# Performance work log

Hardware: AMD Instinct MI355X
Metric: run time of the kernel (lower is better)

## Reference

```python
import jax, jax.numpy as jnp
import numpy as np
from jax import lax

PATCH = 16
DILATIONS = (1, 2, 4, 8)
R2_THRESH = 0.5


def setup_inputs() -> dict:
    key = jax.random.key(0)
    k1, k2, k3 = jax.random.split(key, 3)
    seasonal = jax.random.normal(k1, (32, 2048, 8), dtype=jnp.float32)
    # 4 Conv1d(1,1,k=16) kernels + biases (PyTorch default init scale ~1/sqrt(k))
    conv_w = jax.random.normal(k2, (4, PATCH), dtype=jnp.float32) / np.sqrt(PATCH).astype(np.float32)
    conv_b = jax.random.normal(k3, (4,), dtype=jnp.float32) * 0.01
    return {"seasonal": seasonal, "conv_w": conv_w, "conv_b": conv_b}


def _r2(y):
    n = y.shape[-1]
    x = jnp.arange(n, dtype=y.dtype)
    xm = x - x.mean()                                  # [2p]
    ym = y - y.mean(axis=-1, keepdims=True)            # [..., 2p]
    sxy = jnp.einsum('...k,k->...', ym, xm)
    sxx = jnp.sum(xm * xm)
    syy = jnp.sum(ym * ym, axis=-1)
    return (sxy * sxy) / (sxx * syy)


def _forward(seasonal, conv_w, conv_b):
    B, S, C = seasonal.shape
    p = PATCH
    # channels are processed independently with the SAME convs -> fuse B and C
    x = seasonal.transpose(0, 2, 1).reshape(B * C, 1, S)  # [BC,1,S]
    win = jnp.arange(S - p + 1)[:, None] + jnp.arange(p)[None, :]  # [n_patches,p]
    cand_list = []
    for i, d in enumerate(DILATIONS):
        pad = (p - 1) * d
        out = lax.conv_general_dilated(
            x, conv_w[i].reshape(1, 1, p), window_strides=(1,),
            padding=[(pad, pad)], rhs_dilation=(d,)) + conv_b[i]
        out = out[:, 0, :S]                      # crop to seq_len, [BC,S]
        cand_list.append(out[:, win])            # sliding windows [BC,n_patches,p]
    cand = jnp.concatenate(cand_list, axis=1)    # [BC,N,p]
    N = cand.shape[1]

    # r^2 score for every adjacent pair (vectorized; greedy scan only gates it)
    pair = jnp.concatenate([cand[:, :-1], cand[:, 1:]], axis=-1)  # [BC,N-1,2p]
    can_merge = jnp.pad(_r2(pair) >= R2_THRESH, ((0, 0), (0, 1)),
                        constant_values=False)   # [BC,N]; last idx never merges

    # greedy sequential merge: if pair (i,i+1) merges, i+1 is consumed
    def step(consumed, cm_i):
        merge = jnp.logical_and(~consumed, cm_i)
        return merge, (merge, ~consumed)

    def scan_one(cm):
        _, (merge, valid) = lax.scan(step, jnp.zeros((), jnp.bool_), cm)
        return merge, valid

    merge, valid = jax.vmap(scan_one)(can_merge)  # [BC,N] each

    nxt = jnp.concatenate([cand[:, 1:], cand[:, -1:]], axis=1)
    outs = jnp.where(merge[..., None], 0.5 * (cand + nxt), cand)  # [BC,N,p]

    # pack selected patches to the front (stable order), zero-pad the tail
    order = jnp.argsort(~valid, axis=1)  # jax argsort is stable; valid first
    packed = jnp.take_along_axis(outs, order[..., None], axis=1)
    vmask = jnp.take_along_axis(valid, order, axis=1)
    packed = packed * vmask[..., None].astype(packed.dtype)

    return packed.reshape(B, C, N, p).transpose(0, 2, 3, 1)  # [B,N,p,C]


def reference(seasonal, conv_w, conv_b):
    return _forward(seasonal, conv_w, conv_b)
```

## Files before the change

### kernel.cpp

```cpp
#include <hip/hip_runtime.h>

#define SLEN 2048
#define PATCH 16
#define ND 4
#define NW 2033
#define NCAND 8132
#define NROWS 256
#define NCH 8
#define ROWPAD 8192


__global__ __launch_bounds__(256) void k_conv(
    const float* __restrict__ seasonal,
    const float* __restrict__ conv_w,
    const float* __restrict__ conv_b,
    double* __restrict__ convd,
    float* __restrict__ convf)
{
    const int bid = blockIdx.x;
    const int row = bid >> 2;
    const int d   = bid & 3;
    const int dil = 1 << d;
    const int b = row >> 3, c = row & 7;

    __shared__ float xs[SLEN];
    #pragma unroll
    for (int j = 0; j < SLEN/256; ++j) {
        int s = threadIdx.x + j*256;
        xs[s] = seasonal[(size_t)(b*SLEN + s)*NCH + c];
    }
    double w[PATCH];
    #pragma unroll
    for (int k = 0; k < PATCH; ++k) w[k] = (double)conv_w[d*PATCH + k];
    const double bias = (double)conv_b[d];
    __syncthreads();

    const size_t obase = ((size_t)row*ND + d)*SLEN;
    #pragma unroll
    for (int j = 0; j < SLEN/256; ++j) {
        int t = threadIdx.x + j*256;
        double acc = 0.0;
        #pragma unroll
        for (int k = 0; k < PATCH; ++k) {
            int idx = t - (PATCH-1-k)*dil;
            if (idx >= 0) acc += w[k] * (double)xs[idx];
        }
        acc += bias;
        convd[obase + t] = acc;
        convf[obase + t] = (float)acc;
    }
}

__global__ __launch_bounds__(256) void k_cm(
    const double* __restrict__ convd,
    unsigned char* __restrict__ cmb)
{
    const int row = blockIdx.x >> 2;
    const int d   = blockIdx.x & 3;
    const int tid = threadIdx.x;
    const double* g = convd + ((size_t)row*ND + d)*SLEN;
    unsigned char* crow = cmb + (size_t)row*ROWPAD + d*NW;

    if (tid < 254) {
        const int w0 = tid*8;
        double W1=0.0, W2=0.0, Wk=0.0;
        #pragma unroll
        for (int k = 0; k < 16; ++k) {
            double v = g[w0+k];
            W1 += v; W2 = fma(v,v,W2); Wk = fma((double)k,v,Wk);
        }
        unsigned char bits[8];
        #pragma unroll
        for (int j = 0; j < 8; ++j) {
            double v0 = g[w0+j], v16 = g[w0+j+16];
            double nW1 = W1 + (v16 - v0);
            double nW2 = W2 + (v16*v16 - v0*v0);
            double nWk = Wk - W1 + v0 + 15.0*v16;
            double S1  = W1 + nW1;
            double S2  = W2 + nW2;
            double Sxy = (Wk - 15.5*W1) + (nWk + 0.5*nW1);
            double syy = S2 - S1*S1*(1.0/32.0);
            bits[j] = (unsigned char)((Sxy*Sxy >= 1364.0*syy) && (syy > 0.0));
            W1 = nW1; W2 = nW2; Wk = nWk;
        }
        #pragma unroll
        for (int j = 0; j < 8; ++j) crow[w0+j] = bits[j];
    } else if (tid == 254 && d < 3) {
        const double* g2 = convd + ((size_t)row*ND + d + 1)*SLEN;
        double aW1=0,aW2=0,aWk=0, bW1=0,bW2=0,bWk=0;
        #pragma unroll
        for (int k = 0; k < 16; ++k) {
            double va = g[2032+k]; aW1 += va; aW2 = fma(va,va,aW2); aWk = fma((double)k,va,aWk);
            double vb = g2[k];     bW1 += vb; bW2 = fma(vb,vb,bW2); bWk = fma((double)k,vb,bWk);
        }
        double S1  = aW1 + bW1;
        double S2  = aW2 + bW2;
        double Sxy = (aWk - 15.5*aW1) + (bWk + 0.5*bW1);
        double syy = S2 - S1*S1*(1.0/32.0);
        crow[2032] = (unsigned char)((Sxy*Sxy >= 1364.0*syy) && (syy > 0.0));
    }
}

__global__ __launch_bounds__(256) void k_pack(
    const unsigned char* __restrict__ cmb,
    int* __restrict__ sel)
{
    const int row = blockIdx.x;
    const int tid = threadIdx.x;
    __shared__ unsigned char c0out[256];
    __shared__ int pmax[256];
    __shared__ unsigned sums[256];

    const unsigned* cmw = (const unsigned*)(cmb + (size_t)row*ROWPAD);
    unsigned cmbits = 0;
    #pragma unroll
    for (int q = 0; q < 8; ++q) {
        unsigned wrd = cmw[tid*8 + q];
        #pragma unroll
        for (int bb = 0; bb < 4; ++bb) {
            int p = tid*32 + q*4 + bb;
            unsigned bit = ((wrd >> (8*bb)) & 0xffu) ? 1u : 0u;
            if (p >= NCAND-1) bit = 0;
            cmbits |= bit << (q*4 + bb);
        }
    }

    unsigned inv = ~cmbits;
    unsigned T = (inv == 0u) ? 32u : (unsigned)__clz(inv);
    c0out[tid] = (unsigned char)(T & 1u);
    pmax[tid]  = (inv == 0u) ? -1 : tid;
    __syncthreads();
    for (int off = 1; off < 256; off <<= 1) {
        int v = (tid >= off) ? pmax[tid-off] : -1;
        __syncthreads();
        if (v > pmax[tid]) pmax[tid] = v;
        __syncthreads();
    }
    unsigned carry = 0;
    if (tid > 0) { int m = pmax[tid-1]; if (m >= 0) carry = c0out[m]; }

    unsigned cons = carry;
    unsigned validb = 0, mergeb = 0;
    int cnt = 0;
    const int base = tid*32;
    int nelem = NCAND - base; if (nelem > 32) nelem = 32; if (nelem < 0) nelem = 0;
    for (int w = 0; w < nelem; ++w) {
        unsigned bit = (cmbits >> w) & 1u;
        unsigned val = cons ^ 1u;
        unsigned mrg = bit & val;
        validb |= val << w;
        mergeb |= mrg << w;
        cnt += (int)val;
        cons = mrg;
    }

    sums[tid] = (unsigned)cnt;
    __syncthreads();
    for (int off = 1; off < 256; off <<= 1) {
        unsigned v = (tid >= off) ? sums[tid-off] : 0u;
        __syncthreads();
        sums[tid] += v;
        __syncthreads();
    }
    unsigned r = sums[tid] - (unsigned)cnt;
    unsigned total = sums[255];
    int* selrow = sel + (size_t)row*ROWPAD;
    for (int w = 0; w < nelem; ++w) {
        if ((validb >> w) & 1u)
            selrow[r++] = ((base + w) << 1) | (int)((mergeb >> w) & 1u);
    }
    for (int idx = (int)total + tid; idx < ROWPAD; idx += 256)
        selrow[idx] = -1;
}

__global__ __launch_bounds__(256) void k_out(
    const float* __restrict__ convf,
    const int* __restrict__ sel,
    float* __restrict__ out)
{
    __shared__ float tile[32*132];
    const int t = threadIdx.x;
    const int c = t & 7;
    const int s = t >> 3;
    const unsigned slab = blockIdx.x*32u + (unsigned)s;
    const unsigned b = slab / NCAND;
    const unsigned n = slab - b*NCAND;
    const unsigned row = b*NCH + (unsigned)c;

    const int e = sel[(size_t)row*ROWPAD + n];
    float vals[16];
    if (e < 0) {
        #pragma unroll
        for (int k = 0; k < 16; ++k) vals[k] = 0.0f;
    } else {
        const int i = e >> 1;
        const int d = (i >= 3*NW) ? 3 : (i >= 2*NW) ? 2 : (i >= NW) ? 1 : 0;
        const float* cf = convf + (size_t)row*8192 + i + 15*d;
        float f[17];
        #pragma unroll
        for (int k = 0; k < 17; ++k) f[k] = cf[k];
        if (e & 1) {
            const int i2 = i + 1;
            const int d2 = (i2 >= 3*NW) ? 3 : (i2 >= 2*NW) ? 2 : (i2 >= NW) ? 1 : 0;
            if (d2 != d) {
                const float* cg = convf + (size_t)row*8192 + i2 + 15*d2;
                #pragma unroll
                for (int k = 0; k < 16; ++k) vals[k] = 0.5f*(f[k] + cg[k]);
            } else {
                #pragma unroll
                for (int k = 0; k < 16; ++k) vals[k] = 0.5f*(f[k] + f[k+1]);
            }
        } else {
            #pragma unroll
            for (int k = 0; k < 16; ++k) vals[k] = f[k];
        }
    }
    float* tr = tile + s*132 + c;
    #pragma unroll
    for (int k = 0; k < 16; ++k) tr[k*8] = vals[k];
    __syncthreads();

    const size_t obase = (size_t)blockIdx.x * 4096;
    #pragma unroll
    for (int m = 0; m < 4; ++m) {
        int L  = (t + m*256)*4;
        int s2 = L >> 7, j = L & 127;
        float4 v = *(const float4*)&tile[s2*132 + j];
        *(float4*)&out[obase + L] = v;
    }
}

extern "C" void kernel_launch(void* const* d_in, const int* in_sizes, int n_in,
                              void* d_out, int out_size, void* d_ws, size_t ws_size,
                              hipStream_t stream) {
    const float* seasonal = (const float*)d_in[0];
    const float* conv_w   = (const float*)d_in[1];
    const float* conv_b   = (const float*)d_in[2];
    float* out = (float*)d_out;

    char* ws = (char*)d_ws;
    double*        convd = (double*)(ws);
    float*         convf = (float*)(ws + 16777216);
    unsigned char* cmb   = (unsigned char*)(ws + 25165824);
    int*           sel   = (int*)(ws);

    hipLaunchKernelGGL(k_conv, dim3(NROWS*ND), dim3(256), 0, stream,
                       seasonal, conv_w, conv_b, convd, convf);
    hipLaunchKernelGGL(k_cm,   dim3(NROWS*ND), dim3(256), 0, stream,
                       convd, cmb);
    hipLaunchKernelGGL(k_pack, dim3(NROWS), dim3(256), 0, stream,
                       cmb, sel);
    hipLaunchKernelGGL(k_out,  dim3(8132), dim3(256), 0, stream,
                       convf, sel, out);
}
```

Before: 177.8 us.

## Fuse conv, r2 mask and pack kernels into one per-row front kernel

Merges the convolution, the r^2 merge-flag computation and the greedy pack scan into a single kernel with one block per row. The double-precision conv output now stays in padded shared memory instead of a global buffer, and the byte mask also lives in shared memory. This drops two launches and the global double and byte-mask round trips. In exchange the grid shrinks from 1024 to 256 blocks, so each block runs the four dilations one after another with more syncs and much more shared memory, which may lower occupancy.

```diff
diff --git a/kernel.cpp b/kernel.cpp
--- a/kernel.cpp
+++ b/kernel.cpp
@@ -10,108 +10,99 @@
 #define ROWPAD 8192
 
 
-__global__ __launch_bounds__(256) void k_conv(
+#define CDI5(x) ((x) + ((x) >> 5))
+
+__global__ __launch_bounds__(256) void k_front(
     const float* __restrict__ seasonal,
     const float* __restrict__ conv_w,
     const float* __restrict__ conv_b,
-    double* __restrict__ convd,
-    float* __restrict__ convf)
-{
-    const int bid = blockIdx.x;
-    const int row = bid >> 2;
-    const int d   = bid & 3;
-    const int dil = 1 << d;
-    const int b = row >> 3, c = row & 7;
-
-    __shared__ float xs[SLEN];
-    #pragma unroll
-    for (int j = 0; j < SLEN/256; ++j) {
-        int s = threadIdx.x + j*256;
-        xs[s] = seasonal[(size_t)(b*SLEN + s)*NCH + c];
-    }
-    double w[PATCH];
-    #pragma unroll
-    for (int k = 0; k < PATCH; ++k) w[k] = (double)conv_w[d*PATCH + k];
-    const double bias = (double)conv_b[d];
-    __syncthreads();
-
-    const size_t obase = ((size_t)row*ND + d)*SLEN;
-    #pragma unroll
-    for (int j = 0; j < SLEN/256; ++j) {
-        int t = threadIdx.x + j*256;
-        double acc = 0.0;
-        #pragma unroll
-        for (int k = 0; k < PATCH; ++k) {
-            int idx = t - (PATCH-1-k)*dil;
-            if (idx >= 0) acc += w[k] * (double)xs[idx];
-        }
-        acc += bias;
-        convd[obase + t] = acc;
-        convf[obase + t] = (float)acc;
-    }
-}
-
-__global__ __launch_bounds__(256) void k_cm(
-    const double* __restrict__ convd,
-    unsigned char* __restrict__ cmb)
-{
-    const int row = blockIdx.x >> 2;
-    const int d   = blockIdx.x & 3;
-    const int tid = threadIdx.x;
-    const double* g = convd + ((size_t)row*ND + d)*SLEN;
-    unsigned char* crow = cmb + (size_t)row*ROWPAD + d*NW;
-
-    if (tid < 254) {
-        const int w0 = tid*8;
-        double W1=0.0, W2=0.0, Wk=0.0;
-        #pragma unroll
-        for (int k = 0; k < 16; ++k) {
-            double v = g[w0+k];
-            W1 += v; W2 = fma(v,v,W2); Wk = fma((double)k,v,Wk);
-        }
-        unsigned char bits[8];
-        #pragma unroll
-        for (int j = 0; j < 8; ++j) {
-            double v0 = g[w0+j], v16 = g[w0+j+16];
-            double nW1 = W1 + (v16 - v0);
-            double nW2 = W2 + (v16*v16 - v0*v0);
-            double nWk = Wk - W1 + v0 + 15.0*v16;
-            double S1  = W1 + nW1;
-            double S2  = W2 + nW2;
-            double Sxy = (Wk - 15.5*W1) + (nWk + 0.5*nW1);
-            double syy = S2 - S1*S1*(1.0/32.0);
-            bits[j] = (unsigned char)((Sxy*Sxy >= 1364.0*syy) && (syy > 0.0));
-            W1 = nW1; W2 = nW2; Wk = nWk;
-        }
-        #pragma unroll
-        for (int j = 0; j < 8; ++j) crow[w0+j] = bits[j];
-    } else if (tid == 254 && d < 3) {
-        const double* g2 = convd + ((size_t)row*ND + d + 1)*SLEN;
-        double aW1=0,aW2=0,aWk=0, bW1=0,bW2=0,bWk=0;
-        #pragma unroll
-        for (int k = 0; k < 16; ++k) {
-            double va = g[2032+k]; aW1 += va; aW2 = fma(va,va,aW2); aWk = fma((double)k,va,aWk);
-            double vb = g2[k];     bW1 += vb; bW2 = fma(vb,vb,bW2); bWk = fma((double)k,vb,bWk);
-        }
-        double S1  = aW1 + bW1;
-        double S2  = aW2 + bW2;
-        double Sxy = (aWk - 15.5*aW1) + (bWk + 0.5*bW1);
-        double syy = S2 - S1*S1*(1.0/32.0);
-        crow[2032] = (unsigned char)((Sxy*Sxy >= 1364.0*syy) && (syy > 0.0));
-    }
-}
-
-__global__ __launch_bounds__(256) void k_pack(
-    const unsigned char* __restrict__ cmb,
+    float* __restrict__ convf,
     int* __restrict__ sel)
 {
     const int row = blockIdx.x;
+    const int b = row >> 3, c = row & 7;
     const int tid = threadIdx.x;
+
+    __shared__ float xs[SLEN];
+    __shared__ double cdd[CDI5(SLEN-1)+1];
+    __shared__ double prevtail[16];
+    __shared__ unsigned char cma[8192];
     __shared__ unsigned char c0out[256];
     __shared__ int pmax[256];
     __shared__ unsigned sums[256];
 
-    const unsigned* cmw = (const unsigned*)(cmb + (size_t)row*ROWPAD);
+    #pragma unroll
+    for (int j = 0; j < 8; ++j) {
+        int s = tid + j*256;
+        xs[s] = seasonal[(size_t)(b*SLEN + s)*NCH + c];
+    }
+    __syncthreads();
+
+    for (int d = 0; d < ND; ++d) {
+        double w[PATCH];
+        #pragma unroll
+        for (int k = 0; k < PATCH; ++k) w[k] = (double)conv_w[d*PATCH + k];
+        const double bias = (double)conv_b[d];
+        const int dil = 1 << d;
+        #pragma unroll
+        for (int j = 0; j < 8; ++j) {
+            int t = tid + j*256;
+            double acc = 0.0;
+            #pragma unroll
+            for (int k = 0; k < PATCH; ++k) {
+                int idx = t - (PATCH-1-k)*dil;
+                if (idx >= 0) acc += w[k] * (double)xs[idx];
+            }
+            acc += bias;
+            cdd[CDI5(t)] = acc;
+            convf[(size_t)row*8192 + d*SLEN + t] = (float)acc;
+        }
+        __syncthreads();
+
+        if (tid < 254) {
+            const int w0 = tid*8;
+            double W1=0.0, W2=0.0, Wk=0.0;
+            #pragma unroll
+            for (int k = 0; k < 16; ++k) {
+                double v = cdd[CDI5(w0+k)];
+                W1 += v; W2 = fma(v,v,W2); Wk = fma((double)k,v,Wk);
+            }
+            unsigned char* crow = cma + d*NW;
+            #pragma unroll
+            for (int j = 0; j < 8; ++j) {
+                double v0 = cdd[CDI5(w0+j)], v16 = cdd[CDI5(w0+j+16)];
+                double nW1 = W1 + (v16 - v0);
+                double nW2 = W2 + (v16*v16 - v0*v0);
+                double nWk = Wk - W1 + v0 + 15.0*v16;
+                double S1  = W1 + nW1;
+                double S2  = W2 + nW2;
+                double Sxy = (Wk - 15.5*W1) + (nWk + 0.5*nW1);
+                double syy = S2 - S1*S1*(1.0/32.0);
+                crow[w0+j] = (unsigned char)((Sxy*Sxy >= 1364.0*syy) && (syy > 0.0));
+                W1 = nW1; W2 = nW2; Wk = nWk;
+            }
+        } else if (tid == 255 && d > 0) {
+            double aW1=0,aW2=0,aWk=0, bW1=0,bW2=0,bWk=0;
+            #pragma unroll
+            for (int k = 0; k < 16; ++k) {
+                double va = prevtail[k];
+                double vb = cdd[CDI5(k)];
+                aW1 += va; aW2 = fma(va,va,aW2); aWk = fma((double)k,va,aWk);
+                bW1 += vb; bW2 = fma(vb,vb,bW2); bWk = fma((double)k,vb,bWk);
+            }
+            double S1  = aW1 + bW1;
+            double S2  = aW2 + bW2;
+            double Sxy = (aWk - 15.5*aW1) + (bWk + 0.5*bW1);
+            double syy = S2 - S1*S1*(1.0/32.0);
+            cma[(d-1)*NW + 2032] = (unsigned char)((Sxy*Sxy >= 1364.0*syy) && (syy > 0.0));
+        }
+        __syncthreads();
+
+        if (tid < 16) prevtail[tid] = cdd[CDI5(2032 + tid)];
+        __syncthreads();
+    }
+
+    const unsigned* cmw = (const unsigned*)cma;
     unsigned cmbits = 0;
     #pragma unroll
     for (int q = 0; q < 8; ++q) {
@@ -239,17 +230,11 @@
     float* out = (float*)d_out;
 
     char* ws = (char*)d_ws;
-    double*        convd = (double*)(ws);
-    float*         convf = (float*)(ws + 16777216);
-    unsigned char* cmb   = (unsigned char*)(ws + 25165824);
-    int*           sel   = (int*)(ws);
-
-    hipLaunchKernelGGL(k_conv, dim3(NROWS*ND), dim3(256), 0, stream,
-                       seasonal, conv_w, conv_b, convd, convf);
-    hipLaunchKernelGGL(k_cm,   dim3(NROWS*ND), dim3(256), 0, stream,
-                       convd, cmb);
-    hipLaunchKernelGGL(k_pack, dim3(NROWS), dim3(256), 0, stream,
-                       cmb, sel);
-    hipLaunchKernelGGL(k_out,  dim3(8132), dim3(256), 0, stream,
+    int*   sel   = (int*)(ws);
+    float* convf = (float*)(ws + 16777216);
+
+    hipLaunchKernelGGL(k_front, dim3(NROWS), dim3(256), 0, stream,
+                       seasonal, conv_w, conv_b, convf, sel);
+    hipLaunchKernelGGL(k_out,   dim3(8132), dim3(256), 0, stream,
                        convf, sel, out);
 }
```

Measured after the change: 188.9 us. 1.06x slower.
